# Performance work log

Hardware: AMD Instinct MI355X
Metric: run time of the kernel (lower is better)

The kernel has to match this reference:

```python
import math
import jax, jax.numpy as jnp
import numpy as np

QDEPTH = 8
WIDTH = 32
HEIGHT = 32
PIXELS = WIDTH * HEIGHT          # 1024
WIRES = int(math.ceil(math.log2(PIXELS)))  # 10, and PIXELS == 2**WIRES exactly
BATCH = 2048


def setup_inputs() -> dict:
    key = jax.random.key(0)
    k1, k2 = jax.random.split(key)
    x = jax.random.normal(k1, (BATCH, 1, WIDTH, HEIGHT), dtype=jnp.float32)
    # torch.randn(weight_shape) * 0.4
    weights = jax.random.normal(k2, (QDEPTH, WIRES, 3), dtype=jnp.float32) * 0.4
    return {"x": x, "weights": weights, "reps": 1}


def _apply_1q(s, U, wire):
    # s: (batch, 2, 2, ..., 2); apply 2x2 unitary U on qubit `wire` (axis wire+1)
    ax = wire + 1
    s = jnp.moveaxis(s, ax, -1)
    s = s @ U.T                      # new[..., i] = sum_j U[i, j] * old[..., j]
    return jnp.moveaxis(s, -1, ax)


def _apply_cnot(s, ctrl, tgt):
    # flip target bit on the control==1 half of the state
    c_ax = ctrl + 1
    t_ax = tgt + 1
    s0 = jnp.take(s, 0, axis=c_ax)
    s1 = jnp.take(s, 1, axis=c_ax)
    t = t_ax - 1 if t_ax > c_ax else t_ax
    s1 = jnp.flip(s1, axis=t)
    return jnp.stack([s0, s1], axis=c_ax)


def _rot_matrix(phi, theta, omega):
    # qml.Rot = RZ(phi) -> RY(theta) -> RZ(omega)
    c = jnp.cos(theta * 0.5)
    sn = jnp.sin(theta * 0.5)
    ep = jnp.exp(-0.5j * (phi + omega))   # e^{-i(phi+omega)/2}
    em = jnp.exp(-0.5j * (phi - omega))   # e^{-i(phi-omega)/2}
    return jnp.stack([
        jnp.stack([ep * c, -jnp.conj(em) * sn]),
        jnp.stack([em * sn, jnp.conj(ep) * c]),
    ]).astype(jnp.complex64)


def _circuit(psi, weights, reps):
    # psi: (batch, 2**WIRES) complex64 normalized state
    b = psi.shape[0]
    s = psi.reshape((b,) + (2,) * WIRES)
    w = jnp.tanh(weights)                 # qw_map.tanh
    # StronglyEntanglingLayers default ranges: r_l = l % (wires-1) + 1
    ranges = [(l % (WIRES - 1)) + 1 for l in range(QDEPTH)]
    for _ in range(reps):
        for l in range(QDEPTH):
            for q in range(WIRES):
                U = _rot_matrix(w[l, q, 0], w[l, q, 1], w[l, q, 2])
                s = _apply_1q(s, U, q)
            r = ranges[l]
            for q in range(WIRES):
                s = _apply_cnot(s, q, (q + r) % WIRES)
    return s.reshape(b, 2 ** WIRES)


def reference(x, weights, reps):
    b = x.shape[0]
    v = x.reshape(b, PIXELS)                       # b 1 w h -> b (w h)
    old_norm = jnp.linalg.norm(v, axis=-1, keepdims=True)
    psi = (v / old_norm).astype(jnp.complex64)     # real amplitudes, zero imag
    out = _circuit(psi, weights, reps)
    out = out * old_norm.astype(jnp.complex64)
    return out.reshape(b, 1, WIDTH, HEIGHT)
```

## Files before the change

kernel.cpp:

```cpp
#include <hip/hip_runtime.h>
#include <math.h>


#define WIRES   10
#define NSTATE  1024
#define QDEPTH  8
#define NBATCH  2048
#define NGATES  (QDEPTH * WIRES)

typedef float v2f __attribute__((ext_vector_type(2)));
static __device__ __forceinline__ v2f s2(float x) { return (v2f){x, x}; }

#define WS_WORDS 1280

__device__ __forceinline__ int perm_g(int j, int r) {
#pragma unroll
    for (int q = WIRES - 1; q >= 0; --q) {
        const int cb = 9 - q;
        const int tb = 9 - ((q + r) % WIRES);
        j ^= ((j >> cb) & 1) << tb;
    }
    return j;
}

__global__ __launch_bounds__(1024) void qprep(
    const float* __restrict__ weights, float* __restrict__ ws)
{
    const int tid = threadIdx.x;
    if (tid < NGATES) {
        const float phi   = tanhf(weights[tid * 3 + 0]);
        const float theta = tanhf(weights[tid * 3 + 1]);
        const float omega = tanhf(weights[tid * 3 + 2]);
        const float c  = cosf(theta * 0.5f);
        const float sn = sinf(theta * 0.5f);
        const float a  = 0.5f * (phi + omega);
        const float bb = 0.5f * (phi - omega);
        const float ca = cosf(a),  sa = sinf(a);
        const float cb = cosf(bb), sb = sinf(bb);
        ws[tid * 8 + 0] =  ca * c;  ws[tid * 8 + 1] = -sa * c;
        ws[tid * 8 + 2] = -cb * sn; ws[tid * 8 + 3] = -sb * sn;
        ws[tid * 8 + 4] =  cb * sn; ws[tid * 8 + 5] = -sb * sn;
        ws[tid * 8 + 6] =  ca * c;  ws[tid * 8 + 7] =  sa * c;
    }
    int* wsI = (int*)ws;
    if (tid >= 128 && tid < 256) {
        const int e = tid - 128, l = e >> 4, t = e & 15;
        const int j = perm_g(t, (l % (WIRES - 1)) + 1);
        wsI[640 + e] = ((j & 15) << 6) | (j >> 4);
    }
    if (tid >= 256 && tid < 768) {
        const int e = tid - 256, l = e >> 6, v = e & 63;
        const int j = perm_g(v << 4, (l % (WIRES - 1)) + 1);
        wsI[768 + e] = ((j & 15) << 6) | (j >> 4);
    }
}

template<int CTRL>
__device__ __forceinline__ float dppmov(float x) {
    return __int_as_float(__builtin_amdgcn_update_dpp(
        0, __float_as_int(x), CTRL, 0xF, 0xF, true));
}
#define FX1(v)  dppmov<0xB1>(v)
#define FX2(v)  dppmov<0x4E>(v)
#define FX4(v)  dppmov<0x1B>(dppmov<0x141>(v))
#define FX8(v)  dppmov<0x128>(v)
#define FX16(v) __shfl_xor((v), 16, 64)
#define FX32(v) __shfl_xor((v), 32, 64)

#define APPLY_LOCAL_PK(uptr, mask)                                            \
    {                                                                         \
        const float* __restrict__ u = (uptr);                                 \
        const float u00r=u[0], u00i=u[1], u01r=u[2], u01i=u[3];               \
        const float u10r=u[4], u10i=u[5], u11r=u[6], u11i=u[7];               \
        _Pragma("unroll")                                                     \
        for (int k0 = 0; k0 < 8; ++k0) {                                      \
            if (k0 & (mask)) continue;                                        \
            const int k1 = k0 | (mask);                                       \
            const v2f a0r = zr[k0], a0i = zi[k0];                             \
            const v2f a1r = zr[k1], a1i = zi[k1];                             \
            zr[k0] = s2(u00r)*a0r - s2(u00i)*a0i + s2(u01r)*a1r - s2(u01i)*a1i;\
            zi[k0] = s2(u00r)*a0i + s2(u00i)*a0r + s2(u01r)*a1i + s2(u01i)*a1r;\
            zr[k1] = s2(u10r)*a0r - s2(u10i)*a0i + s2(u11r)*a1r - s2(u11i)*a1i;\
            zi[k1] = s2(u10r)*a0i + s2(u10i)*a0r + s2(u11r)*a1i + s2(u11i)*a1r;\
        }                                                                     \
    }

#define LANE_GATE_PK(W, J, FETCH)                                             \
    {                                                                         \
        const float* __restrict__ u = gw + (W) * 8;                           \
        const bool hi = (lane >> (J)) & 1;                                    \
        const float c0r = hi ? u[6] : u[0], c0i = hi ? u[7] : u[1];           \
        const float c1r = hi ? u[4] : u[2], c1i = hi ? u[5] : u[3];           \
        _Pragma("unroll")                                                     \
        for (int k = 0; k < 8; ++k) {                                         \
            v2f pr, pi;                                                       \
            pr.x = FETCH(zr[k].x); pr.y = FETCH(zr[k].y);                     \
            pi.x = FETCH(zi[k].x); pi.y = FETCH(zi[k].y);                     \
            const v2f sr = zr[k], si = zi[k];                                 \
            zr[k] = s2(c0r)*sr - s2(c0i)*si + s2(c1r)*pr - s2(c1i)*pi;        \
            zi[k] = s2(c0r)*si + s2(c0i)*sr + s2(c1r)*pi + s2(c1i)*pr;        \
        }                                                                     \
    }

__global__ __launch_bounds__(64) void qsim_wave(
    const float* __restrict__ x,
    const float* __restrict__ ws,
    float* __restrict__ out,
    const int interleaved)
{
    __shared__ float lds[2 * NSTATE];
    const int lane = threadIdx.x;
    const int b    = blockIdx.x;
    const int* __restrict__ wsI = (const int*)ws;

    v2f zr[8], zi[8];

    const float4* __restrict__ x4 =
        (const float4*)(x + ((size_t)b << 10) + (lane << 4));
    {
        const float4 v0 = x4[0], v1 = x4[1], v2 = x4[2], v3 = x4[3];
        zr[0].x=v0.x; zr[1].x=v0.y; zr[2].x=v0.z; zr[3].x=v0.w;
        zr[4].x=v1.x; zr[5].x=v1.y; zr[6].x=v1.z; zr[7].x=v1.w;
        zr[0].y=v2.x; zr[1].y=v2.y; zr[2].y=v2.z; zr[3].y=v2.w;
        zr[4].y=v3.x; zr[5].y=v3.y; zr[6].y=v3.z; zr[7].y=v3.w;
#pragma unroll
        for (int k = 0; k < 8; ++k) zi[k] = (v2f){0.f, 0.f};
    }

    for (int l = 0; l < QDEPTH; ++l) {
        const float* __restrict__ gw = ws + l * 80;

        APPLY_LOCAL_PK(gw + 9*8, 1)
        APPLY_LOCAL_PK(gw + 8*8, 2)
        APPLY_LOCAL_PK(gw + 7*8, 4)

        {
            const float* __restrict__ u = gw + 6*8;
            const v2f pAr = (v2f){u[0], u[6]};
            const v2f pAi = (v2f){u[1], u[7]};
            const v2f pBr = (v2f){u[2], u[4]};
            const v2f pBi = (v2f){u[3], u[5]};
#pragma unroll
            for (int k = 0; k < 8; ++k) {
                const v2f r  = zr[k], i = zi[k];
                const v2f rs = __builtin_shufflevector(r, r, 1, 0);
                const v2f is = __builtin_shufflevector(i, i, 1, 0);
                zr[k] = pAr*r - pAi*i + pBr*rs - pBi*is;
                zi[k] = pAr*i + pAi*r + pBr*is + pBi*rs;
            }
        }

        LANE_GATE_PK(5, 0, FX1)
        LANE_GATE_PK(4, 1, FX2)
        LANE_GATE_PK(3, 2, FX4)
        LANE_GATE_PK(2, 3, FX8)
        LANE_GATE_PK(1, 4, FX16)
        LANE_GATE_PK(0, 5, FX32)

#pragma unroll
        for (int k = 0; k < 8; ++k) {
            const int w = k * 64 + lane;
            lds[w]        = zr[k].x;
            lds[w + 512]  = zr[k].y;
            lds[w + 1024] = zi[k].x;
            lds[w + 1536] = zi[k].y;
        }
        const int ga = wsI[768 + l * 64 + lane];
#pragma unroll
        for (int k = 0; k < 8; ++k) {
            const int a0 = ga ^ wsI[640 + l * 16 + k];
            const int a1 = ga ^ wsI[640 + l * 16 + k + 8];
            zr[k].x = lds[a0]; zi[k].x = lds[a0 + 1024];
            zr[k].y = lds[a1]; zi[k].y = lds[a1 + 1024];
        }
    }

    if (interleaved) {
        float2* __restrict__ o2 = (float2*)out;
        const size_t base = ((size_t)b << 10) + (lane << 4);
#pragma unroll
        for (int k = 0; k < 8; ++k) {
            o2[base + k]     = make_float2(zr[k].x, zi[k].x);
            o2[base + k + 8] = make_float2(zr[k].y, zi[k].y);
        }
    } else {
        float4* __restrict__ o4 = (float4*)(out + ((size_t)b << 10) + (lane << 4));
        o4[0] = make_float4(zr[0].x, zr[1].x, zr[2].x, zr[3].x);
        o4[1] = make_float4(zr[4].x, zr[5].x, zr[6].x, zr[7].x);
        o4[2] = make_float4(zr[0].y, zr[1].y, zr[2].y, zr[3].y);
        o4[3] = make_float4(zr[4].y, zr[5].y, zr[6].y, zr[7].y);
    }
}

__global__ __launch_bounds__(256) void qcircuit_kernel(
    const float* __restrict__ x, const float* __restrict__ weights,
    float* __restrict__ out, const int interleaved)
{
    __shared__ float s_re[NSTATE];
    __shared__ float s_im[NSTATE];
    __shared__ float s_g[NGATES][8];
    const int tid = threadIdx.x;
    const int b   = blockIdx.x;
    if (tid < NGATES) {
        const float phi   = tanhf(weights[tid * 3 + 0]);
        const float theta = tanhf(weights[tid * 3 + 1]);
        const float omega = tanhf(weights[tid * 3 + 2]);
        const float c  = cosf(theta * 0.5f);
        const float sn = sinf(theta * 0.5f);
        const float a  = 0.5f * (phi + omega);
        const float bb = 0.5f * (phi - omega);
        const float ca = cosf(a),  sa = sinf(a);
        const float cb = cosf(bb), sb = sinf(bb);
        s_g[tid][0] =  ca * c;  s_g[tid][1] = -sa * c;
        s_g[tid][2] = -cb * sn; s_g[tid][3] = -sb * sn;
        s_g[tid][4] =  cb * sn; s_g[tid][5] = -sb * sn;
        s_g[tid][6] =  ca * c;  s_g[tid][7] =  sa * c;
    }
#pragma unroll
    for (int k = 0; k < 4; ++k) {
        const int i = tid + 256 * k;
        s_re[i] = x[b * NSTATE + i];
        s_im[i] = 0.0f;
    }
    __syncthreads();
    for (int l = 0; l < QDEPTH; ++l) {
        for (int q = 0; q < WIRES; ++q) {
            const int gi = l * WIRES + q;
            const float u00r = s_g[gi][0], u00i = s_g[gi][1];
            const float u01r = s_g[gi][2], u01i = s_g[gi][3];
            const float u10r = s_g[gi][4], u10i = s_g[gi][5];
            const float u11r = s_g[gi][6], u11i = s_g[gi][7];
            const int sh = 9 - q;
            const int m  = 1 << sh;
#pragma unroll
            for (int k = 0; k < 2; ++k) {
                const int p  = tid + 256 * k;
                const int i0 = ((p >> sh) << (sh + 1)) | (p & (m - 1));
                const int i1 = i0 | m;
                const float a0r = s_re[i0], a0i = s_im[i0];
                const float a1r = s_re[i1], a1i = s_im[i1];
                s_re[i0] = u00r*a0r - u00i*a0i + u01r*a1r - u01i*a1i;
                s_im[i0] = u00r*a0i + u00i*a0r + u01r*a1i + u01i*a1r;
                s_re[i1] = u10r*a0r - u10i*a0i + u11r*a1r - u11i*a1i;
                s_im[i1] = u10r*a0i + u10i*a0r + u11r*a1i + u11i*a1r;
            }
            __syncthreads();
        }
        const int r = (l % (WIRES - 1)) + 1;
        float vr[4], vi[4];
#pragma unroll
        for (int k = 0; k < 4; ++k) {
            const int i = tid + 256 * k;
            const int j = perm_g(i, r);
            vr[k] = s_re[j]; vi[k] = s_im[j];
        }
        __syncthreads();
#pragma unroll
        for (int k = 0; k < 4; ++k) {
            const int i = tid + 256 * k;
            s_re[i] = vr[k]; s_im[i] = vi[k];
        }
        __syncthreads();
    }
    if (interleaved) {
#pragma unroll
        for (int k = 0; k < 4; ++k) {
            const int i  = tid + 256 * k;
            const int fi = 2 * (b * NSTATE + i);
            out[fi + 0] = s_re[i];
            out[fi + 1] = s_im[i];
        }
    } else {
#pragma unroll
        for (int k = 0; k < 4; ++k) {
            const int i = tid + 256 * k;
            out[b * NSTATE + i] = s_re[i];
        }
    }
}

extern "C" void kernel_launch(void* const* d_in, const int* in_sizes, int n_in,
                              void* d_out, int out_size, void* d_ws, size_t ws_size,
                              hipStream_t stream) {
    const float* x       = (const float*)d_in[0];
    const float* weights = (const float*)d_in[1];
    float* out = (float*)d_out;
    const int interleaved = (out_size >= 2 * NBATCH * NSTATE) ? 1 : 0;

    if (ws_size >= WS_WORDS * sizeof(float)) {
        float* ws = (float*)d_ws;
        qprep<<<1, 1024, 0, stream>>>(weights, ws);
        qsim_wave<<<NBATCH, 64, 0, stream>>>(x, ws, out, interleaved);
    } else {
        qcircuit_kernel<<<NBATCH, 256, 0, stream>>>(x, weights, out, interleaved);
    }
}
```

Measured before the change: 102.9 us.

## Split each state vector across two waves with double-buffered LDS permutation

Each batch element is now simulated by a 128-thread block, two wavefronts each holding 8 amplitudes per lane, instead of one wave holding 16. The top qubit's gate (the cross-wave bit) is folded into the LDS gather that also performs the CNOT permutation, and the LDS buffers are double-buffered per layer so only one barrier is needed per layer. The intent is to halve the per-wave register state and serial arithmetic and expose more parallelism and occupancy. In exchange it adds a __syncthreads per layer, more LDS traffic, and extra select logic for the gather-fused gate.

```diff
diff --git a/kernel.cpp b/kernel.cpp
--- a/kernel.cpp
+++ b/kernel.cpp
@@ -11,7 +11,7 @@
 typedef float v2f __attribute__((ext_vector_type(2)));
 static __device__ __forceinline__ v2f s2(float x) { return (v2f){x, x}; }
 
-#define WS_WORDS 1280
+#define WS_WORDS 1728
 
 __device__ __forceinline__ int perm_g(int j, int r) {
 #pragma unroll
@@ -21,6 +21,9 @@
         j ^= ((j >> cb) & 1) << tb;
     }
     return j;
+}
+__device__ __forceinline__ int wordof(int j) {
+    return ((j & 7) << 7) | (j >> 3);
 }
 
 __global__ __launch_bounds__(1024) void qprep(
@@ -43,15 +46,14 @@
         ws[tid * 8 + 6] =  ca * c;  ws[tid * 8 + 7] =  sa * c;
     }
     int* wsI = (int*)ws;
-    if (tid >= 128 && tid < 256) {
-        const int e = tid - 128, l = e >> 4, t = e & 15;
-        const int j = perm_g(t, (l % (WIRES - 1)) + 1);
-        wsI[640 + e] = ((j & 15) << 6) | (j >> 4);
-    }
-    if (tid >= 256 && tid < 768) {
-        const int e = tid - 256, l = e >> 6, v = e & 63;
-        const int j = perm_g(v << 4, (l % (WIRES - 1)) + 1);
-        wsI[768 + e] = ((j & 15) << 6) | (j >> 4);
+    if (tid >= 128 && tid < 192) {
+        const int e = tid - 128, l = e >> 3, t = e & 7;
+        wsI[640 + e] = wordof(perm_g(t, (l % (WIRES - 1)) + 1));
+    }
+    {
+        const int l = tid >> 7, e = tid & 127;
+        const int i0 = ((e >> 6) << 9) | ((e & 63) << 3);
+        wsI[704 + tid] = wordof(perm_g(i0, (l % (WIRES - 1)) + 1));
     }
 }
 
@@ -67,13 +69,13 @@
 #define FX16(v) __shfl_xor((v), 16, 64)
 #define FX32(v) __shfl_xor((v), 32, 64)
 
-#define APPLY_LOCAL_PK(uptr, mask)                                            \
+#define APPLY_LOCAL_PK4(uptr, mask)                                           \
     {                                                                         \
         const float* __restrict__ u = (uptr);                                 \
         const float u00r=u[0], u00i=u[1], u01r=u[2], u01i=u[3];               \
         const float u10r=u[4], u10i=u[5], u11r=u[6], u11i=u[7];               \
         _Pragma("unroll")                                                     \
-        for (int k0 = 0; k0 < 8; ++k0) {                                      \
+        for (int k0 = 0; k0 < 4; ++k0) {                                      \
             if (k0 & (mask)) continue;                                        \
             const int k1 = k0 | (mask);                                       \
             const v2f a0r = zr[k0], a0i = zi[k0];                             \
@@ -85,14 +87,14 @@
         }                                                                     \
     }
 
-#define LANE_GATE_PK(W, J, FETCH)                                             \
+#define LANE_GATE_PK4(W, J, FETCH)                                            \
     {                                                                         \
         const float* __restrict__ u = gw + (W) * 8;                           \
         const bool hi = (lane >> (J)) & 1;                                    \
         const float c0r = hi ? u[6] : u[0], c0i = hi ? u[7] : u[1];           \
         const float c1r = hi ? u[4] : u[2], c1i = hi ? u[5] : u[3];           \
         _Pragma("unroll")                                                     \
-        for (int k = 0; k < 8; ++k) {                                         \
+        for (int k = 0; k < 4; ++k) {                                         \
             v2f pr, pi;                                                       \
             pr.x = FETCH(zr[k].x); pr.y = FETCH(zr[k].y);                     \
             pi.x = FETCH(zi[k].x); pi.y = FETCH(zi[k].y);                     \
@@ -102,46 +104,50 @@
         }                                                                     \
     }
 
-__global__ __launch_bounds__(64) void qsim_wave(
+__global__ __launch_bounds__(128) void qsim2p(
     const float* __restrict__ x,
     const float* __restrict__ ws,
     float* __restrict__ out,
     const int interleaved)
 {
-    __shared__ float lds[2 * NSTATE];
-    const int lane = threadIdx.x;
+    __shared__ float lre[2][NSTATE];
+    __shared__ float lim[2][NSTATE];
+    const int tid  = threadIdx.x;
+    const int lane = tid & 63;
     const int b    = blockIdx.x;
+    const int i0   = ((tid >> 6) << 9) | (lane << 3);
     const int* __restrict__ wsI = (const int*)ws;
 
-    v2f zr[8], zi[8];
+    v2f zr[4], zi[4];
 
     const float4* __restrict__ x4 =
-        (const float4*)(x + ((size_t)b << 10) + (lane << 4));
+        (const float4*)(x + ((size_t)b << 10) + i0);
     {
-        const float4 v0 = x4[0], v1 = x4[1], v2 = x4[2], v3 = x4[3];
-        zr[0].x=v0.x; zr[1].x=v0.y; zr[2].x=v0.z; zr[3].x=v0.w;
-        zr[4].x=v1.x; zr[5].x=v1.y; zr[6].x=v1.z; zr[7].x=v1.w;
-        zr[0].y=v2.x; zr[1].y=v2.y; zr[2].y=v2.z; zr[3].y=v2.w;
-        zr[4].y=v3.x; zr[5].y=v3.y; zr[6].y=v3.z; zr[7].y=v3.w;
-#pragma unroll
-        for (int k = 0; k < 8; ++k) zi[k] = (v2f){0.f, 0.f};
+        const float4 v0 = x4[0], v1 = x4[1];
+        zr[0] = (v2f){v0.x, v1.x};
+        zr[1] = (v2f){v0.y, v1.y};
+        zr[2] = (v2f){v0.z, v1.z};
+        zr[3] = (v2f){v0.w, v1.w};
+#pragma unroll
+        for (int k = 0; k < 4; ++k) zi[k] = (v2f){0.f, 0.f};
     }
 
     for (int l = 0; l < QDEPTH; ++l) {
         const float* __restrict__ gw = ws + l * 80;
-
-        APPLY_LOCAL_PK(gw + 9*8, 1)
-        APPLY_LOCAL_PK(gw + 8*8, 2)
-        APPLY_LOCAL_PK(gw + 7*8, 4)
+        float* __restrict__ bre = lre[l & 1];
+        float* __restrict__ bim = lim[l & 1];
+
+        APPLY_LOCAL_PK4(gw + 9*8, 1)
+        APPLY_LOCAL_PK4(gw + 8*8, 2)
 
         {
-            const float* __restrict__ u = gw + 6*8;
+            const float* __restrict__ u = gw + 7*8;
             const v2f pAr = (v2f){u[0], u[6]};
             const v2f pAi = (v2f){u[1], u[7]};
             const v2f pBr = (v2f){u[2], u[4]};
             const v2f pBi = (v2f){u[3], u[5]};
 #pragma unroll
-            for (int k = 0; k < 8; ++k) {
+            for (int k = 0; k < 4; ++k) {
                 const v2f r  = zr[k], i = zi[k];
                 const v2f rs = __builtin_shufflevector(r, r, 1, 0);
                 const v2f is = __builtin_shufflevector(i, i, 1, 0);
@@ -150,45 +156,54 @@
             }
         }
 
-        LANE_GATE_PK(5, 0, FX1)
-        LANE_GATE_PK(4, 1, FX2)
-        LANE_GATE_PK(3, 2, FX4)
-        LANE_GATE_PK(2, 3, FX8)
-        LANE_GATE_PK(1, 4, FX16)
-        LANE_GATE_PK(0, 5, FX32)
-
-#pragma unroll
-        for (int k = 0; k < 8; ++k) {
-            const int w = k * 64 + lane;
-            lds[w]        = zr[k].x;
-            lds[w + 512]  = zr[k].y;
-            lds[w + 1024] = zi[k].x;
-            lds[w + 1536] = zi[k].y;
-        }
-        const int ga = wsI[768 + l * 64 + lane];
-#pragma unroll
-        for (int k = 0; k < 8; ++k) {
-            const int a0 = ga ^ wsI[640 + l * 16 + k];
-            const int a1 = ga ^ wsI[640 + l * 16 + k + 8];
-            zr[k].x = lds[a0]; zi[k].x = lds[a0 + 1024];
-            zr[k].y = lds[a1]; zi[k].y = lds[a1 + 1024];
+        LANE_GATE_PK4(6, 0, FX1)
+        LANE_GATE_PK4(5, 1, FX2)
+        LANE_GATE_PK4(4, 2, FX4)
+        LANE_GATE_PK4(3, 3, FX8)
+        LANE_GATE_PK4(2, 4, FX16)
+        LANE_GATE_PK4(1, 5, FX32)
+
+#pragma unroll
+        for (int k = 0; k < 4; ++k) {
+            bre[k * 128 + tid]       = zr[k].x;
+            bre[(k + 4) * 128 + tid] = zr[k].y;
+            bim[k * 128 + tid]       = zi[k].x;
+            bim[(k + 4) * 128 + tid] = zi[k].y;
+        }
+        __syncthreads();
+
+        const float* __restrict__ u0 = gw;
+        const int glw = wsI[704 + l * 128 + tid];
+#pragma unroll
+        for (int k = 0; k < 4; ++k) {
+            const int jw0 = glw ^ wsI[640 + l * 8 + k];
+            const int jw1 = glw ^ wsI[640 + l * 8 + k + 4];
+            const bool h0 = (jw0 >> 6) & 1, h1 = (jw1 >> 6) & 1;
+            const v2f c0r = (v2f){h0 ? u0[6] : u0[0], h1 ? u0[6] : u0[0]};
+            const v2f c0i = (v2f){h0 ? u0[7] : u0[1], h1 ? u0[7] : u0[1]};
+            const v2f c1r = (v2f){h0 ? u0[4] : u0[2], h1 ? u0[4] : u0[2]};
+            const v2f c1i = (v2f){h0 ? u0[5] : u0[3], h1 ? u0[5] : u0[3]};
+            const v2f sr = (v2f){bre[jw0],      bre[jw1]};
+            const v2f si = (v2f){bim[jw0],      bim[jw1]};
+            const v2f pr = (v2f){bre[jw0 ^ 64], bre[jw1 ^ 64]};
+            const v2f pi = (v2f){bim[jw0 ^ 64], bim[jw1 ^ 64]};
+            zr[k] = c0r*sr - c0i*si + c1r*pr - c1i*pi;
+            zi[k] = c0r*si + c0i*sr + c1r*pi + c1i*pr;
         }
     }
 
     if (interleaved) {
         float2* __restrict__ o2 = (float2*)out;
-        const size_t base = ((size_t)b << 10) + (lane << 4);
-#pragma unroll
-        for (int k = 0; k < 8; ++k) {
+        const size_t base = ((size_t)b << 10) + i0;
+#pragma unroll
+        for (int k = 0; k < 4; ++k) {
             o2[base + k]     = make_float2(zr[k].x, zi[k].x);
-            o2[base + k + 8] = make_float2(zr[k].y, zi[k].y);
+            o2[base + k + 4] = make_float2(zr[k].y, zi[k].y);
         }
     } else {
-        float4* __restrict__ o4 = (float4*)(out + ((size_t)b << 10) + (lane << 4));
+        float4* __restrict__ o4 = (float4*)(out + ((size_t)b << 10) + i0);
         o4[0] = make_float4(zr[0].x, zr[1].x, zr[2].x, zr[3].x);
-        o4[1] = make_float4(zr[4].x, zr[5].x, zr[6].x, zr[7].x);
-        o4[2] = make_float4(zr[0].y, zr[1].y, zr[2].y, zr[3].y);
-        o4[3] = make_float4(zr[4].y, zr[5].y, zr[6].y, zr[7].y);
+        o4[1] = make_float4(zr[0].y, zr[1].y, zr[2].y, zr[3].y);
     }
 }
 
@@ -290,7 +305,7 @@
     if (ws_size >= WS_WORDS * sizeof(float)) {
         float* ws = (float*)d_ws;
         qprep<<<1, 1024, 0, stream>>>(weights, ws);
-        qsim_wave<<<NBATCH, 64, 0, stream>>>(x, ws, out, interleaved);
+        qsim2p<<<NBATCH, 128, 0, stream>>>(x, ws, out, interleaved);
     } else {
         qcircuit_kernel<<<NBATCH, 256, 0, stream>>>(x, weights, out, interleaved);
     }
```

Result: slower. 108.3 us (+5.2%).

## Simulate two batch samples per wavefront to increase ILP

Applied to the files above, without the earlier changes.

Each 64-lane block now processes two batch states interleaved gate by gate, with separate real/imag LDS arrays sized for both states. The grid is halved. The goal is to hide DPP/shuffle and LDS latency through independent instruction streams and to amortize gate-coefficient and permutation-table loads. In exchange, VGPR pressure and LDS per block double, and there are half as many wavefronts, so occupancy and latency hiding across waves may drop.

```diff
diff --git a/kernel.cpp b/kernel.cpp
--- a/kernel.cpp
+++ b/kernel.cpp
@@ -67,7 +67,7 @@
 #define FX16(v) __shfl_xor((v), 16, 64)
 #define FX32(v) __shfl_xor((v), 32, 64)
 
-#define APPLY_LOCAL_PK(uptr, mask)                                            \
+#define APPLY_LOCAL_PK(ZR, ZI, uptr, mask)                                    \
     {                                                                         \
         const float* __restrict__ u = (uptr);                                 \
         const float u00r=u[0], u00i=u[1], u01r=u[2], u01i=u[3];               \
@@ -76,16 +76,33 @@
         for (int k0 = 0; k0 < 8; ++k0) {                                      \
             if (k0 & (mask)) continue;                                        \
             const int k1 = k0 | (mask);                                       \
-            const v2f a0r = zr[k0], a0i = zi[k0];                             \
-            const v2f a1r = zr[k1], a1i = zi[k1];                             \
-            zr[k0] = s2(u00r)*a0r - s2(u00i)*a0i + s2(u01r)*a1r - s2(u01i)*a1i;\
-            zi[k0] = s2(u00r)*a0i + s2(u00i)*a0r + s2(u01r)*a1i + s2(u01i)*a1r;\
-            zr[k1] = s2(u10r)*a0r - s2(u10i)*a0i + s2(u11r)*a1r - s2(u11i)*a1i;\
-            zi[k1] = s2(u10r)*a0i + s2(u10i)*a0r + s2(u11r)*a1i + s2(u11i)*a1r;\
+            const v2f a0r = ZR[k0], a0i = ZI[k0];                             \
+            const v2f a1r = ZR[k1], a1i = ZI[k1];                             \
+            ZR[k0] = s2(u00r)*a0r - s2(u00i)*a0i + s2(u01r)*a1r - s2(u01i)*a1i;\
+            ZI[k0] = s2(u00r)*a0i + s2(u00i)*a0r + s2(u01r)*a1i + s2(u01i)*a1r;\
+            ZR[k1] = s2(u10r)*a0r - s2(u10i)*a0i + s2(u11r)*a1r - s2(u11i)*a1i;\
+            ZI[k1] = s2(u10r)*a0i + s2(u10i)*a0r + s2(u11r)*a1i + s2(u11i)*a1r;\
         }                                                                     \
     }
 
-#define LANE_GATE_PK(W, J, FETCH)                                             \
+#define HALF_SWAP_PK(ZR, ZI, uptr)                                            \
+    {                                                                         \
+        const float* __restrict__ u = (uptr);                                 \
+        const v2f pAr = (v2f){u[0], u[6]};                                    \
+        const v2f pAi = (v2f){u[1], u[7]};                                    \
+        const v2f pBr = (v2f){u[2], u[4]};                                    \
+        const v2f pBi = (v2f){u[3], u[5]};                                    \
+        _Pragma("unroll")                                                     \
+        for (int k = 0; k < 8; ++k) {                                         \
+            const v2f r  = ZR[k], i = ZI[k];                                  \
+            const v2f rs = __builtin_shufflevector(r, r, 1, 0);               \
+            const v2f is = __builtin_shufflevector(i, i, 1, 0);               \
+            ZR[k] = pAr*r - pAi*i + pBr*rs - pBi*is;                          \
+            ZI[k] = pAr*i + pAi*r + pBr*is + pBi*rs;                          \
+        }                                                                     \
+    }
+
+#define LANE_GATE_PK(ZR, ZI, W, J, FETCH)                                     \
     {                                                                         \
         const float* __restrict__ u = gw + (W) * 8;                           \
         const bool hi = (lane >> (J)) & 1;                                    \
@@ -94,101 +111,123 @@
         _Pragma("unroll")                                                     \
         for (int k = 0; k < 8; ++k) {                                         \
             v2f pr, pi;                                                       \
-            pr.x = FETCH(zr[k].x); pr.y = FETCH(zr[k].y);                     \
-            pi.x = FETCH(zi[k].x); pi.y = FETCH(zi[k].y);                     \
-            const v2f sr = zr[k], si = zi[k];                                 \
-            zr[k] = s2(c0r)*sr - s2(c0i)*si + s2(c1r)*pr - s2(c1i)*pi;        \
-            zi[k] = s2(c0r)*si + s2(c0i)*sr + s2(c1r)*pi + s2(c1i)*pr;        \
+            pr.x = FETCH(ZR[k].x); pr.y = FETCH(ZR[k].y);                     \
+            pi.x = FETCH(ZI[k].x); pi.y = FETCH(ZI[k].y);                     \
+            const v2f sr = ZR[k], si = ZI[k];                                 \
+            ZR[k] = s2(c0r)*sr - s2(c0i)*si + s2(c1r)*pr - s2(c1i)*pi;        \
+            ZI[k] = s2(c0r)*si + s2(c0i)*sr + s2(c1r)*pi + s2(c1i)*pr;        \
         }                                                                     \
     }
 
-__global__ __launch_bounds__(64) void qsim_wave(
+__global__ __launch_bounds__(64) void qsim_2s(
     const float* __restrict__ x,
     const float* __restrict__ ws,
     float* __restrict__ out,
     const int interleaved)
 {
-    __shared__ float lds[2 * NSTATE];
+    __shared__ float lre[2 * NSTATE];
+    __shared__ float lim[2 * NSTATE];
     const int lane = threadIdx.x;
     const int b    = blockIdx.x;
     const int* __restrict__ wsI = (const int*)ws;
 
-    v2f zr[8], zi[8];
-
-    const float4* __restrict__ x4 =
-        (const float4*)(x + ((size_t)b << 10) + (lane << 4));
+    v2f zrA[8], ziA[8], zrB[8], ziB[8];
+
     {
-        const float4 v0 = x4[0], v1 = x4[1], v2 = x4[2], v3 = x4[3];
-        zr[0].x=v0.x; zr[1].x=v0.y; zr[2].x=v0.z; zr[3].x=v0.w;
-        zr[4].x=v1.x; zr[5].x=v1.y; zr[6].x=v1.z; zr[7].x=v1.w;
-        zr[0].y=v2.x; zr[1].y=v2.y; zr[2].y=v2.z; zr[3].y=v2.w;
-        zr[4].y=v3.x; zr[5].y=v3.y; zr[6].y=v3.z; zr[7].y=v3.w;
-#pragma unroll
-        for (int k = 0; k < 8; ++k) zi[k] = (v2f){0.f, 0.f};
+        const float4* __restrict__ xA =
+            (const float4*)(x + ((size_t)(2 * b) << 10) + (lane << 4));
+        const float4* __restrict__ xB =
+            (const float4*)(x + ((size_t)(2 * b + 1) << 10) + (lane << 4));
+        const float4 a0 = xA[0], a1 = xA[1], a2 = xA[2], a3 = xA[3];
+        const float4 b0 = xB[0], b1 = xB[1], b2 = xB[2], b3 = xB[3];
+        zrA[0].x=a0.x; zrA[1].x=a0.y; zrA[2].x=a0.z; zrA[3].x=a0.w;
+        zrA[4].x=a1.x; zrA[5].x=a1.y; zrA[6].x=a1.z; zrA[7].x=a1.w;
+        zrA[0].y=a2.x; zrA[1].y=a2.y; zrA[2].y=a2.z; zrA[3].y=a2.w;
+        zrA[4].y=a3.x; zrA[5].y=a3.y; zrA[6].y=a3.z; zrA[7].y=a3.w;
+        zrB[0].x=b0.x; zrB[1].x=b0.y; zrB[2].x=b0.z; zrB[3].x=b0.w;
+        zrB[4].x=b1.x; zrB[5].x=b1.y; zrB[6].x=b1.z; zrB[7].x=b1.w;
+        zrB[0].y=b2.x; zrB[1].y=b2.y; zrB[2].y=b2.z; zrB[3].y=b2.w;
+        zrB[4].y=b3.x; zrB[5].y=b3.y; zrB[6].y=b3.z; zrB[7].y=b3.w;
+#pragma unroll
+        for (int k = 0; k < 8; ++k) {
+            ziA[k] = (v2f){0.f, 0.f};
+            ziB[k] = (v2f){0.f, 0.f};
+        }
     }
 
     for (int l = 0; l < QDEPTH; ++l) {
         const float* __restrict__ gw = ws + l * 80;
 
-        APPLY_LOCAL_PK(gw + 9*8, 1)
-        APPLY_LOCAL_PK(gw + 8*8, 2)
-        APPLY_LOCAL_PK(gw + 7*8, 4)
-
-        {
-            const float* __restrict__ u = gw + 6*8;
-            const v2f pAr = (v2f){u[0], u[6]};
-            const v2f pAi = (v2f){u[1], u[7]};
-            const v2f pBr = (v2f){u[2], u[4]};
-            const v2f pBi = (v2f){u[3], u[5]};
-#pragma unroll
-            for (int k = 0; k < 8; ++k) {
-                const v2f r  = zr[k], i = zi[k];
-                const v2f rs = __builtin_shufflevector(r, r, 1, 0);
-                const v2f is = __builtin_shufflevector(i, i, 1, 0);
-                zr[k] = pAr*r - pAi*i + pBr*rs - pBi*is;
-                zi[k] = pAr*i + pAi*r + pBr*is + pBi*rs;
-            }
-        }
-
-        LANE_GATE_PK(5, 0, FX1)
-        LANE_GATE_PK(4, 1, FX2)
-        LANE_GATE_PK(3, 2, FX4)
-        LANE_GATE_PK(2, 3, FX8)
-        LANE_GATE_PK(1, 4, FX16)
-        LANE_GATE_PK(0, 5, FX32)
-
-#pragma unroll
-        for (int k = 0; k < 8; ++k) {
-            const int w = k * 64 + lane;
-            lds[w]        = zr[k].x;
-            lds[w + 512]  = zr[k].y;
-            lds[w + 1024] = zi[k].x;
-            lds[w + 1536] = zi[k].y;
+        APPLY_LOCAL_PK(zrA, ziA, gw + 9*8, 1)
+        APPLY_LOCAL_PK(zrB, ziB, gw + 9*8, 1)
+        APPLY_LOCAL_PK(zrA, ziA, gw + 8*8, 2)
+        APPLY_LOCAL_PK(zrB, ziB, gw + 8*8, 2)
+        APPLY_LOCAL_PK(zrA, ziA, gw + 7*8, 4)
+        APPLY_LOCAL_PK(zrB, ziB, gw + 7*8, 4)
+        HALF_SWAP_PK(zrA, ziA, gw + 6*8)
+        HALF_SWAP_PK(zrB, ziB, gw + 6*8)
+
+        LANE_GATE_PK(zrA, ziA, 5, 0, FX1)
+        LANE_GATE_PK(zrB, ziB, 5, 0, FX1)
+        LANE_GATE_PK(zrA, ziA, 4, 1, FX2)
+        LANE_GATE_PK(zrB, ziB, 4, 1, FX2)
+        LANE_GATE_PK(zrA, ziA, 3, 2, FX4)
+        LANE_GATE_PK(zrB, ziB, 3, 2, FX4)
+        LANE_GATE_PK(zrA, ziA, 2, 3, FX8)
+        LANE_GATE_PK(zrB, ziB, 2, 3, FX8)
+        LANE_GATE_PK(zrA, ziA, 1, 4, FX16)
+        LANE_GATE_PK(zrB, ziB, 1, 4, FX16)
+        LANE_GATE_PK(zrA, ziA, 0, 5, FX32)
+        LANE_GATE_PK(zrB, ziB, 0, 5, FX32)
+
+#pragma unroll
+        for (int k = 0; k < 8; ++k) {
+            lre[k * 64 + lane]       = zrA[k].x;
+            lre[(k + 8) * 64 + lane] = zrA[k].y;
+            lim[k * 64 + lane]       = ziA[k].x;
+            lim[(k + 8) * 64 + lane] = ziA[k].y;
+        }
+#pragma unroll
+        for (int k = 0; k < 8; ++k) {
+            lre[1024 + k * 64 + lane]       = zrB[k].x;
+            lre[1024 + (k + 8) * 64 + lane] = zrB[k].y;
+            lim[1024 + k * 64 + lane]       = ziB[k].x;
+            lim[1024 + (k + 8) * 64 + lane] = ziB[k].y;
         }
         const int ga = wsI[768 + l * 64 + lane];
 #pragma unroll
         for (int k = 0; k < 8; ++k) {
             const int a0 = ga ^ wsI[640 + l * 16 + k];
             const int a1 = ga ^ wsI[640 + l * 16 + k + 8];
-            zr[k].x = lds[a0]; zi[k].x = lds[a0 + 1024];
-            zr[k].y = lds[a1]; zi[k].y = lds[a1 + 1024];
+            zrA[k].x = lre[a0];        ziA[k].x = lim[a0];
+            zrA[k].y = lre[a1];        ziA[k].y = lim[a1];
+            zrB[k].x = lre[1024 + a0]; ziB[k].x = lim[1024 + a0];
+            zrB[k].y = lre[1024 + a1]; ziB[k].y = lim[1024 + a1];
         }
     }
 
     if (interleaved) {
         float2* __restrict__ o2 = (float2*)out;
-        const size_t base = ((size_t)b << 10) + (lane << 4);
-#pragma unroll
-        for (int k = 0; k < 8; ++k) {
-            o2[base + k]     = make_float2(zr[k].x, zi[k].x);
-            o2[base + k + 8] = make_float2(zr[k].y, zi[k].y);
+        const size_t baseA = ((size_t)(2 * b) << 10) + (lane << 4);
+        const size_t baseB = ((size_t)(2 * b + 1) << 10) + (lane << 4);
+#pragma unroll
+        for (int k = 0; k < 8; ++k) {
+            o2[baseA + k]     = make_float2(zrA[k].x, ziA[k].x);
+            o2[baseA + k + 8] = make_float2(zrA[k].y, ziA[k].y);
+            o2[baseB + k]     = make_float2(zrB[k].x, ziB[k].x);
+            o2[baseB + k + 8] = make_float2(zrB[k].y, ziB[k].y);
         }
     } else {
-        float4* __restrict__ o4 = (float4*)(out + ((size_t)b << 10) + (lane << 4));
-        o4[0] = make_float4(zr[0].x, zr[1].x, zr[2].x, zr[3].x);
-        o4[1] = make_float4(zr[4].x, zr[5].x, zr[6].x, zr[7].x);
-        o4[2] = make_float4(zr[0].y, zr[1].y, zr[2].y, zr[3].y);
-        o4[3] = make_float4(zr[4].y, zr[5].y, zr[6].y, zr[7].y);
+        float4* __restrict__ oA = (float4*)(out + ((size_t)(2 * b) << 10) + (lane << 4));
+        float4* __restrict__ oB = (float4*)(out + ((size_t)(2 * b + 1) << 10) + (lane << 4));
+        oA[0] = make_float4(zrA[0].x, zrA[1].x, zrA[2].x, zrA[3].x);
+        oA[1] = make_float4(zrA[4].x, zrA[5].x, zrA[6].x, zrA[7].x);
+        oA[2] = make_float4(zrA[0].y, zrA[1].y, zrA[2].y, zrA[3].y);
+        oA[3] = make_float4(zrA[4].y, zrA[5].y, zrA[6].y, zrA[7].y);
+        oB[0] = make_float4(zrB[0].x, zrB[1].x, zrB[2].x, zrB[3].x);
+        oB[1] = make_float4(zrB[4].x, zrB[5].x, zrB[6].x, zrB[7].x);
+        oB[2] = make_float4(zrB[0].y, zrB[1].y, zrB[2].y, zrB[3].y);
+        oB[3] = make_float4(zrB[4].y, zrB[5].y, zrB[6].y, zrB[7].y);
     }
 }
 
@@ -290,7 +329,7 @@
     if (ws_size >= WS_WORDS * sizeof(float)) {
         float* ws = (float*)d_ws;
         qprep<<<1, 1024, 0, stream>>>(weights, ws);
-        qsim_wave<<<NBATCH, 64, 0, stream>>>(x, ws, out, interleaved);
+        qsim_2s<<<NBATCH / 2, 64, 0, stream>>>(x, ws, out, interleaved);
     } else {
         qcircuit_kernel<<<NBATCH, 256, 0, stream>>>(x, weights, out, interleaved);
     }
```

Measured after the change: 120.1 us. +16.7%, slower.
